# Performance work log

Measured on AMD Instinct MI355X. Metric: run time of the kernel, lower is better.

## Reference

```python
import jax, jax.numpy as jnp
import numpy as np

B, L, D = 8, 4096, 2048
E, TOPK, RANK = 8, 2, 8
ALPHA = 1.0 / RANK
LN_EPS = 1e-5


def setup_inputs() -> dict:
    key = jax.random.key(0)
    ks = jax.random.split(key, 7)
    return {
        "x": jax.random.normal(ks[0], (B, L, D), dtype=jnp.float32),
        "gate_w": jax.random.normal(ks[1], (E, D), dtype=jnp.float32) * 0.02,
        "gate_b": jax.random.normal(ks[2], (E,), dtype=jnp.float32) * 0.02,
        "A": jax.random.normal(ks[3], (E, RANK, D), dtype=jnp.float32) * 0.02,
        "Bw": jax.random.normal(ks[4], (E, D, RANK), dtype=jnp.float32) * 0.02,
        "gamma": 1.0 + 0.1 * jax.random.normal(ks[5], (D,), dtype=jnp.float32),
        "beta": 0.1 * jax.random.normal(ks[6], (D,), dtype=jnp.float32),
    }


def reference(x, gate_w, gate_b, A, Bw, gamma, beta):
    # pooled hidden state per sequence: [B, D]
    h = x.mean(axis=1)
    # router (eval mode: no jitter noise)
    logits = h @ gate_w.T + gate_b                 # [B, E]
    vals, idx = jax.lax.top_k(logits, TOPK)        # [B, k]
    w = jax.nn.softmax(vals, axis=-1)              # [B, k]

    # ---- auxiliary losses ----
    counts = jnp.sum(jax.nn.one_hot(idx.reshape(-1), E, dtype=logits.dtype), axis=0)
    f = counts / (logits.shape[0] * TOPK)          # fraction routed to each expert
    P = jax.nn.softmax(logits, axis=-1).mean(axis=0)
    load_balance = E * jnp.sum(f * P)
    z_loss = jnp.mean(jax.nn.logsumexp(logits, axis=-1) ** 2)
    p = f + 1e-8
    p = p / p.sum()
    renyi_loss = jnp.log(jnp.sum(p ** 2))          # -(log(sum p^2)/(1-2))*(-1)
    aux = 0.01 * load_balance + 0.001 * z_loss + 0.01 * renyi_loss

    # ---- sparse LoRA expert dispatch (gather selected experts, tiny rank-8 GEMMs) ----
    A_sel = A[idx]                                 # [B, k, r, D]
    B_sel = Bw[idx]                                # [B, k, D, r]
    t = jnp.einsum('bd,bkrd->bkr', h, A_sel)       # [B, k, r]
    expert_out = jnp.einsum('bkr,bkdr->bkd', t, B_sel)  # [B, k, D]
    delta = jnp.sum(w[..., None] * expert_out, axis=1) * ALPHA  # [B, D]

    # residual add + LayerNorm over feature dim
    y = x + delta[:, None, :]
    mu = y.mean(axis=-1, keepdims=True)
    var = y.var(axis=-1, keepdims=True)
    y = (y - mu) / jnp.sqrt(var + LN_EPS) * gamma + beta
    return y, aux
```

## Files before the change

### kernel.cpp

```cpp
#include <hip/hip_runtime.h>
#include <math.h>

#define NB 8
#define NL 4096
#define ND 2048
#define NE 8
#define KTOP 2
#define NR 8
#define ALPHA 0.125f
#define LN_EPS 1e-5f
#define SPLIT 64

typedef float f32x4 __attribute__((ext_vector_type(4)));

__global__ __launch_bounds__(256) void k1_partial_mean(const float* __restrict__ x,
                                                       float* __restrict__ partial) {
    int bid = blockIdx.x;
    int half = bid & 1;
    int b = (bid >> 1) & (NB - 1);
    int s = bid >> 4;
    const int lchunk = NL / SPLIT;
    int d4 = half * 1024 + threadIdx.x * 4;
    const float* xp = x + ((size_t)(b * NL + s * lchunk)) * ND + d4;
    f32x4 a0 = {0.f, 0.f, 0.f, 0.f}, a1 = a0, a2 = a0, a3 = a0;
    for (int i = 0; i < lchunk; i += 4) {
        f32x4 v0 = *(const f32x4*)(xp + (size_t)(i + 0) * ND);
        f32x4 v1 = *(const f32x4*)(xp + (size_t)(i + 1) * ND);
        f32x4 v2 = *(const f32x4*)(xp + (size_t)(i + 2) * ND);
        f32x4 v3 = *(const f32x4*)(xp + (size_t)(i + 3) * ND);
        a0 += v0; a1 += v1; a2 += v2; a3 += v3;
    }
    f32x4 acc = (a0 + a1) + (a2 + a3);
    *(f32x4*)(partial + ((size_t)(b * SPLIT + s)) * ND + d4) = acc;
}

__global__ __launch_bounds__(256) void kB_router(const float* __restrict__ partial,
                                                 const float* __restrict__ gate_w,
                                                 const float* __restrict__ gate_b,
                                                 const float* __restrict__ A,
                                                 const float* __restrict__ Bw,
                                                 float* __restrict__ delta,
                                                 float* __restrict__ logits_out,
                                                 int* __restrict__ idx_out) {
    __shared__ float sh_h[ND];
    __shared__ float sh_logits[NE];
    __shared__ float sh_t[KTOP * NR];
    __shared__ float sh_w[KTOP];
    __shared__ int sh_idx[KTOP];
    int b = blockIdx.x;
    int tid = threadIdx.x;

    const float* pb = partial + (size_t)b * SPLIT * ND;
    for (int d4 = tid; d4 < ND / 4; d4 += 256) {
        f32x4 s0 = {0.f, 0.f, 0.f, 0.f}, s1 = s0, s2 = s0, s3 = s0;
#pragma unroll 4
        for (int s = 0; s < SPLIT; s += 4) {
            s0 += *(const f32x4*)(pb + (size_t)(s + 0) * ND + d4 * 4);
            s1 += *(const f32x4*)(pb + (size_t)(s + 1) * ND + d4 * 4);
            s2 += *(const f32x4*)(pb + (size_t)(s + 2) * ND + d4 * 4);
            s3 += *(const f32x4*)(pb + (size_t)(s + 3) * ND + d4 * 4);
        }
        f32x4 r = ((s0 + s1) + (s2 + s3)) * (1.0f / NL);
        *(f32x4*)(sh_h + d4 * 4) = r;
    }
    __syncthreads();

    {
        int e = tid >> 5, lane32 = tid & 31;
        const f32x4* gw = (const f32x4*)(gate_w + (size_t)e * ND);
        float p = 0.f;
#pragma unroll 4
        for (int d4 = lane32; d4 < ND / 4; d4 += 32) {
            f32x4 gv = gw[d4];
            f32x4 hv = *(const f32x4*)(sh_h + d4 * 4);
            p += gv.x * hv.x + gv.y * hv.y + gv.z * hv.z + gv.w * hv.w;
        }
        for (int off = 16; off; off >>= 1) p += __shfl_down(p, off);
        if (lane32 == 0) sh_logits[e] = p + gate_b[e];
    }
    __syncthreads();

    if (tid == 0) {
        float v1 = -1e30f; int e1 = 0;
        for (int e = 0; e < NE; ++e) if (sh_logits[e] > v1) { v1 = sh_logits[e]; e1 = e; }
        float v2 = -1e30f; int e2 = 0;
        for (int e = 0; e < NE; ++e) if (e != e1 && sh_logits[e] > v2) { v2 = sh_logits[e]; e2 = e; }
        float ex = expf(v2 - v1);
        float w1 = 1.0f / (1.0f + ex);
        sh_idx[0] = e1; sh_idx[1] = e2;
        sh_w[0] = w1; sh_w[1] = ex * w1;
        idx_out[b * KTOP] = e1; idx_out[b * KTOP + 1] = e2;
        for (int e = 0; e < NE; ++e) logits_out[b * NE + e] = sh_logits[e];
    }
    __syncthreads();

    {
        int grp = tid >> 4, lane16 = tid & 15;
        int k = grp >> 3, r = grp & 7;
        int e = sh_idx[k];
        const f32x4* ap = (const f32x4*)(A + ((size_t)e * NR + r) * ND);
        float p = 0.f;
#pragma unroll 4
        for (int d4 = lane16; d4 < ND / 4; d4 += 16) {
            f32x4 av = ap[d4];
            f32x4 hv = *(const f32x4*)(sh_h + d4 * 4);
            p += av.x * hv.x + av.y * hv.y + av.z * hv.z + av.w * hv.w;
        }
        for (int off = 8; off; off >>= 1) p += __shfl_down(p, off);
        if (lane16 == 0) sh_t[grp] = p;
    }
    __syncthreads();

    for (int dd = tid; dd < ND; dd += 256) {
        float acc = 0.f;
#pragma unroll
        for (int k = 0; k < KTOP; ++k) {
            int e = sh_idx[k];
            const f32x4* bw = (const f32x4*)(Bw + ((size_t)e * ND + dd) * NR);
            f32x4 w0 = bw[0], w1 = bw[1];
            float s = sh_t[k * NR + 0] * w0.x + sh_t[k * NR + 1] * w0.y +
                      sh_t[k * NR + 2] * w0.z + sh_t[k * NR + 3] * w0.w +
                      sh_t[k * NR + 4] * w1.x + sh_t[k * NR + 5] * w1.y +
                      sh_t[k * NR + 6] * w1.z + sh_t[k * NR + 7] * w1.w;
            acc += sh_w[k] * s;
        }
        delta[b * ND + dd] = acc * ALPHA;
    }
}

__global__ void k3_aux(const float* __restrict__ logits, const int* __restrict__ idxp,
                       float* __restrict__ aux_out) {
    if (threadIdx.x != 0 || blockIdx.x != 0) return;
    float counts[NE];
    for (int e = 0; e < NE; ++e) counts[e] = 0.f;
    for (int i = 0; i < NB * KTOP; ++i) counts[idxp[i]] += 1.f;
    float f[NE], P[NE];
    for (int e = 0; e < NE; ++e) { f[e] = counts[e] * (1.0f / (NB * KTOP)); P[e] = 0.f; }
    float z = 0.f;
    for (int b = 0; b < NB; ++b) {
        const float* lg = logits + b * NE;
        float m = lg[0];
        for (int e = 1; e < NE; ++e) m = fmaxf(m, lg[e]);
        float s = 0.f;
        for (int e = 0; e < NE; ++e) s += expf(lg[e] - m);
        float inv = 1.0f / s;
        for (int e = 0; e < NE; ++e) P[e] += expf(lg[e] - m) * inv;
        float lse = m + logf(s);
        z += lse * lse;
    }
    z *= (1.0f / NB);
    float lb = 0.f;
    for (int e = 0; e < NE; ++e) lb += f[e] * (P[e] * (1.0f / NB));
    lb *= (float)NE;
    float psum = 0.f;
    for (int e = 0; e < NE; ++e) psum += f[e] + 1e-8f;
    float s2 = 0.f;
    for (int e = 0; e < NE; ++e) { float p = (f[e] + 1e-8f) / psum; s2 += p * p; }
    float renyi = logf(s2);
    aux_out[0] = 0.01f * lb + 0.001f * z + 0.01f * renyi;
}

__global__ __launch_bounds__(256) void k4_ln(const float* __restrict__ x,
                                             const float* __restrict__ delta,
                                             const float* __restrict__ gamma,
                                             const float* __restrict__ beta,
                                             float* __restrict__ y) {
    int wave = blockIdx.x * 4 + (threadIdx.x >> 6);
    int lane = threadIdx.x & 63;

    f32x4 g[8], be[8];
#pragma unroll
    for (int j = 0; j < 8; ++j) {
        g[j]  = *(const f32x4*)(gamma + (lane + 64 * j) * 4);
        be[j] = *(const f32x4*)(beta  + (lane + 64 * j) * 4);
    }

    for (int row = wave; row < NB * NL; row += 4096) {
        int b = row >> 12;
        const f32x4* xp = (const f32x4*)(x + (size_t)row * ND);
        const f32x4* dp = (const f32x4*)(delta + (size_t)b * ND);
        f32x4 v[8];
#pragma unroll
        for (int j = 0; j < 8; ++j) v[j] = xp[lane + 64 * j];
#pragma unroll
        for (int j = 0; j < 8; ++j) v[j] += dp[lane + 64 * j];

        float s = 0.f, ss = 0.f;
#pragma unroll
        for (int j = 0; j < 8; ++j) {
            s  += v[j].x + v[j].y + v[j].z + v[j].w;
            ss += v[j].x * v[j].x + v[j].y * v[j].y + v[j].z * v[j].z + v[j].w * v[j].w;
        }
        for (int off = 32; off; off >>= 1) {
            s  += __shfl_xor(s, off);
            ss += __shfl_xor(ss, off);
        }
        float mu = s * (1.0f / ND);
        float var = ss * (1.0f / ND) - mu * mu;
        float rstd = rsqrtf(var + LN_EPS);

        f32x4* yp = (f32x4*)(y + (size_t)row * ND);
#pragma unroll
        for (int j = 0; j < 8; ++j) {
            f32x4 o = (v[j] - mu) * rstd * g[j] + be[j];
            __builtin_nontemporal_store(o, yp + lane + 64 * j);
        }
    }
}

extern "C" void kernel_launch(void* const* d_in, const int* in_sizes, int n_in,
                              void* d_out, int out_size, void* d_ws, size_t ws_size,
                              hipStream_t stream) {
    const float* x      = (const float*)d_in[0];
    const float* gate_w = (const float*)d_in[1];
    const float* gate_b = (const float*)d_in[2];
    const float* A      = (const float*)d_in[3];
    const float* Bw     = (const float*)d_in[4];
    const float* gamma  = (const float*)d_in[5];
    const float* beta   = (const float*)d_in[6];
    float* y   = (float*)d_out;
    float* aux = y + (size_t)NB * NL * ND;

    float* partial = (float*)d_ws;
    float* delta   = partial + (size_t)NB * SPLIT * ND;
    float* logits  = delta + NB * ND;
    int*   idxp    = (int*)(logits + NB * NE);

    hipLaunchKernelGGL(k1_partial_mean, dim3(SPLIT * NB * 2), dim3(256), 0, stream,
                       x, partial);
    hipLaunchKernelGGL(kB_router, dim3(NB), dim3(256), 0, stream,
                       partial, gate_w, gate_b, A, Bw, delta, logits, idxp);
    hipLaunchKernelGGL(k3_aux, dim3(1), dim3(64), 0, stream, logits, idxp, aux);
    hipLaunchKernelGGL(k4_ln, dim3(1024), dim3(256), 0, stream,
                       x, delta, gamma, beta, y);
}
```

Baseline: 151.9 us.

## Fuse aux-loss kernel into LayerNorm kernel and assign contiguous rows per wave

Drops the single-thread aux-loss launch and computes the loss in thread 0 of block 0 at the end of the LayerNorm kernel, removing one launch. Each wave now handles 8 contiguous rows of one batch, so the delta vector is loaded once into registers and reused across those rows. Gamma and beta are no longer held in registers; they are reloaded per row, which lowers register pressure. Output stores switch from nontemporal to normal stores, which may change cache behaviour for the 256 MB output write.

```diff
diff --git a/kernel.cpp b/kernel.cpp
--- a/kernel.cpp
+++ b/kernel.cpp
@@ -128,62 +128,33 @@
     }
 }
 
-__global__ void k3_aux(const float* __restrict__ logits, const int* __restrict__ idxp,
-                       float* __restrict__ aux_out) {
-    if (threadIdx.x != 0 || blockIdx.x != 0) return;
-    float counts[NE];
-    for (int e = 0; e < NE; ++e) counts[e] = 0.f;
-    for (int i = 0; i < NB * KTOP; ++i) counts[idxp[i]] += 1.f;
-    float f[NE], P[NE];
-    for (int e = 0; e < NE; ++e) { f[e] = counts[e] * (1.0f / (NB * KTOP)); P[e] = 0.f; }
-    float z = 0.f;
-    for (int b = 0; b < NB; ++b) {
-        const float* lg = logits + b * NE;
-        float m = lg[0];
-        for (int e = 1; e < NE; ++e) m = fmaxf(m, lg[e]);
-        float s = 0.f;
-        for (int e = 0; e < NE; ++e) s += expf(lg[e] - m);
-        float inv = 1.0f / s;
-        for (int e = 0; e < NE; ++e) P[e] += expf(lg[e] - m) * inv;
-        float lse = m + logf(s);
-        z += lse * lse;
-    }
-    z *= (1.0f / NB);
-    float lb = 0.f;
-    for (int e = 0; e < NE; ++e) lb += f[e] * (P[e] * (1.0f / NB));
-    lb *= (float)NE;
-    float psum = 0.f;
-    for (int e = 0; e < NE; ++e) psum += f[e] + 1e-8f;
-    float s2 = 0.f;
-    for (int e = 0; e < NE; ++e) { float p = (f[e] + 1e-8f) / psum; s2 += p * p; }
-    float renyi = logf(s2);
-    aux_out[0] = 0.01f * lb + 0.001f * z + 0.01f * renyi;
-}
-
 __global__ __launch_bounds__(256) void k4_ln(const float* __restrict__ x,
                                              const float* __restrict__ delta,
                                              const float* __restrict__ gamma,
                                              const float* __restrict__ beta,
-                                             float* __restrict__ y) {
+                                             const float* __restrict__ logits,
+                                             const int* __restrict__ idxp,
+                                             float* __restrict__ y,
+                                             float* __restrict__ aux_out) {
     int wave = blockIdx.x * 4 + (threadIdx.x >> 6);
     int lane = threadIdx.x & 63;
-
-    f32x4 g[8], be[8];
-#pragma unroll
-    for (int j = 0; j < 8; ++j) {
-        g[j]  = *(const f32x4*)(gamma + (lane + 64 * j) * 4);
-        be[j] = *(const f32x4*)(beta  + (lane + 64 * j) * 4);
-    }
-
-    for (int row = wave; row < NB * NL; row += 4096) {
-        int b = row >> 12;
-        const f32x4* xp = (const f32x4*)(x + (size_t)row * ND);
-        const f32x4* dp = (const f32x4*)(delta + (size_t)b * ND);
+    int row0 = wave * 8;
+    int b = row0 >> 12;
+
+    const f32x4* dp = (const f32x4*)(delta + (size_t)b * ND);
+    f32x4 d[8];
+#pragma unroll
+    for (int j = 0; j < 8; ++j) d[j] = dp[lane + 64 * j];
+
+#pragma unroll 1
+    for (int k = 0; k < 8; ++k) {
+        size_t base = (size_t)(row0 + k) * ND;
+        const f32x4* xp = (const f32x4*)(x + base);
         f32x4 v[8];
 #pragma unroll
         for (int j = 0; j < 8; ++j) v[j] = xp[lane + 64 * j];
 #pragma unroll
-        for (int j = 0; j < 8; ++j) v[j] += dp[lane + 64 * j];
+        for (int j = 0; j < 8; ++j) v[j] += d[j];
 
         float s = 0.f, ss = 0.f;
 #pragma unroll
@@ -199,12 +170,42 @@
         float var = ss * (1.0f / ND) - mu * mu;
         float rstd = rsqrtf(var + LN_EPS);
 
-        f32x4* yp = (f32x4*)(y + (size_t)row * ND);
+        f32x4* yp = (f32x4*)(y + base);
 #pragma unroll
         for (int j = 0; j < 8; ++j) {
-            f32x4 o = (v[j] - mu) * rstd * g[j] + be[j];
-            __builtin_nontemporal_store(o, yp + lane + 64 * j);
-        }
+            f32x4 gv = *(const f32x4*)(gamma + (lane + 64 * j) * 4);
+            f32x4 bv = *(const f32x4*)(beta  + (lane + 64 * j) * 4);
+            yp[lane + 64 * j] = (v[j] - mu) * rstd * gv + bv;
+        }
+    }
+
+    if (blockIdx.x == 0 && threadIdx.x == 0) {
+        float counts[NE];
+        for (int e = 0; e < NE; ++e) counts[e] = 0.f;
+        for (int i = 0; i < NB * KTOP; ++i) counts[idxp[i]] += 1.f;
+        float f[NE], P[NE];
+        for (int e = 0; e < NE; ++e) { f[e] = counts[e] * (1.0f / (NB * KTOP)); P[e] = 0.f; }
+        float z = 0.f;
+        for (int bb = 0; bb < NB; ++bb) {
+            const float* lg = logits + bb * NE;
+            float m = lg[0];
+            for (int e = 1; e < NE; ++e) m = fmaxf(m, lg[e]);
+            float sum = 0.f;
+            for (int e = 0; e < NE; ++e) sum += expf(lg[e] - m);
+            float inv = 1.0f / sum;
+            for (int e = 0; e < NE; ++e) P[e] += expf(lg[e] - m) * inv;
+            float lse = m + logf(sum);
+            z += lse * lse;
+        }
+        z *= (1.0f / NB);
+        float lb = 0.f;
+        for (int e = 0; e < NE; ++e) lb += f[e] * (P[e] * (1.0f / NB));
+        lb *= (float)NE;
+        float psum = 0.f;
+        for (int e = 0; e < NE; ++e) psum += f[e] + 1e-8f;
+        float s2 = 0.f;
+        for (int e = 0; e < NE; ++e) { float p = (f[e] + 1e-8f) / psum; s2 += p * p; }
+        aux_out[0] = 0.01f * lb + 0.001f * z + 0.01f * logf(s2);
     }
 }
 
@@ -230,7 +231,6 @@
                        x, partial);
     hipLaunchKernelGGL(kB_router, dim3(NB), dim3(256), 0, stream,
                        partial, gate_w, gate_b, A, Bw, delta, logits, idxp);
-    hipLaunchKernelGGL(k3_aux, dim3(1), dim3(64), 0, stream, logits, idxp, aux);
     hipLaunchKernelGGL(k4_ln, dim3(1024), dim3(256), 0, stream,
-                       x, delta, gamma, beta, y);
-}
+                       x, delta, gamma, beta, logits, idxp, y, aux);
+}
```

Measured after the change: 172.3 us. +13.4%, slower.
